# Kernel tuning notes

Hardware: AMD Instinct MI355X
Metric: run time of the kernel (lower is better)

Reference implementation:

```python
import jax, jax.numpy as jnp
import numpy as np
import math

N, L, S, H, E, D = 2, 2048, 2048, 16, 64, 64

def setup_inputs() -> dict:
    key = jax.random.key(0)
    kq, kk, kv = jax.random.split(key, 3)
    return {
        "queries": jax.random.normal(kq, (N, L, H, E), dtype=jnp.float32),
        "keys": jax.random.normal(kk, (N, S, H, E), dtype=jnp.float32),
        "values": jax.random.normal(kv, (N, S, H, D), dtype=jnp.float32),
        "attn_mask": jnp.zeros((L, S), dtype=jnp.float32),  # additive mask
    }

def reference(queries, keys, values, attn_mask):
    e = queries.shape[-1]
    softmax_temp = 1.0 / math.sqrt(e)  # self.softmax_temp is None -> 1/sqrt(E)
    # (N,L,H,E) x (N,S,H,E) -> (N,H,L,S)
    qk = jnp.einsum('nlhe,nshe->nhls', queries, keys)
    qk = qk + attn_mask  # additive mask broadcast over (N,H)
    att = jax.nn.softmax(softmax_temp * qk, axis=-1)
    # dropout rate 0.0 (eval) -> identity
    v = jnp.einsum('nhls,nshd->nlhd', att, values)
    return v
```

## Files before the change

### kernel.cpp

```cpp
#include <hip/hip_runtime.h>
#include <hip/hip_bf16.h>


typedef short bf16x8 __attribute__((ext_vector_type(8)));
typedef short short4v __attribute__((ext_vector_type(4)));
typedef unsigned uint2v __attribute__((ext_vector_type(2)));
typedef unsigned uint4v __attribute__((ext_vector_type(4)));
typedef float f32x4 __attribute__((ext_vector_type(4)));

constexpr int Nb = 2, Lq = 2048, Sk = 2048, Hh = 16, Ee = 64, Dd = 64;
constexpr int BM = 128;
constexpr int BN = 64;
constexpr int NT = Sk / BN;
constexpr int KVB = 4096;
constexpr int MSKB = 2048;
constexpr float SCALE_LOG2E = 0.125f * 1.4426950408889634f;

__device__ __forceinline__ short f2bf(float f) {
  union { float f; unsigned u; } v; v.f = f;
  unsigned r = (v.u + 0x7fffu + ((v.u >> 16) & 1u)) >> 16;
  return (short)r;
}

__device__ __forceinline__ unsigned pack_bf16x2(float a, float b) {
  union { __hip_bfloat162 h; unsigned u; } v;
  float2 f; f.x = a; f.y = b;
  v.h = __float22bfloat162_rn(f);
  return v.u;
}

__device__ __forceinline__ float bf_lo(unsigned u) { return __uint_as_float(u << 16); }
__device__ __forceinline__ float bf_hi(unsigned u) { return __uint_as_float(u & 0xffff0000u); }

__device__ __forceinline__ void async_copy16(const void* g, void* l) {
  __builtin_amdgcn_global_load_lds(
      (const __attribute__((address_space(1))) unsigned int*)g,
      (__attribute__((address_space(3))) unsigned int*)l, 16, 0, 0);
}

__global__ __launch_bounds__(256) void prep_all(const float* __restrict__ K,
                                                const float* __restrict__ V,
                                                const float* __restrict__ M,
                                                short* __restrict__ KVf,
                                                short* __restrict__ Mg) {
  if (blockIdx.x < KVB) {
    int gid = blockIdx.x * 256 + threadIdx.x;
    int off8 = gid & 1023;
    int t  = (gid >> 10) & 31;
    int nh = gid >> 15;
    int n = nh >> 4, h = nh & 15;
    short* dst = KVf + ((size_t)(nh * NT + t)) * 8192 + off8 * 8;
    if (off8 < 512) {
      int ch = off8 >> 6;
      int l  = off8 & 63;
      int sb = ch >> 1, kc = ch & 1, c = l & 15, quad = l >> 4;
      const float* p = K + (((size_t)n * Sk + (t * 64 + sb * 16 + c)) * Hh + h) * Ee
                         + kc * 32 + quad * 8;
      float4 x = *(const float4*)(p);
      float4 y = *(const float4*)(p + 4);
      bf16x8 o;
      o[0] = f2bf(x.x); o[1] = f2bf(x.y); o[2] = f2bf(x.z); o[3] = f2bf(x.w);
      o[4] = f2bf(y.x); o[5] = f2bf(y.y); o[6] = f2bf(y.z); o[7] = f2bf(y.w);
      *(bf16x8*)dst = o;
    } else {
      int pos = off8 - 512;
      int chunk = pos >> 6;
      int l = pos & 63;
      int db = chunk >> 1, sbp = chunk & 1, cc = l & 15, quad = l >> 4;
      const float* pbase = V + (((size_t)n * Sk + (t * 64 + sbp * 32 + quad * 4)) * Hh + h) * Dd
                             + db * 16 + cc;
      bf16x8 o;
#pragma unroll
      for (int k = 0; k < 8; ++k) {
        int s_off = (k >> 2) * 16 + (k & 3);
        o[k] = f2bf(pbase[(size_t)s_off * Hh * Dd]);
      }
      *(bf16x8*)dst = o;
    }
  } else {
    int u = (blockIdx.x - KVB) * 256 + threadIdx.x;
    int sub  = u & 3;
    int lane = (u >> 2) & 63;
    int t    = (u >> 8) & 31;
    int qw   = u >> 13;
    int cb = sub >> 1, sbp = sub & 1;
    int c = lane & 15, quad = lane >> 4;
    int row = (qw >> 2) * 128 + (qw & 3) * 32 + cb * 16 + c;
    short o[8];
#pragma unroll
    for (int k = 0; k < 2; ++k) {
      int sb = sbp * 2 + k;
      float4 mv = *(const float4*)(M + (size_t)row * Sk + t * 64 + sb * 16 + quad * 4);
      o[k * 4 + 0] = f2bf(mv.x * SCALE_LOG2E);
      o[k * 4 + 1] = f2bf(mv.y * SCALE_LOG2E);
      o[k * 4 + 2] = f2bf(mv.z * SCALE_LOG2E);
      o[k * 4 + 3] = f2bf(mv.w * SCALE_LOG2E);
    }
    *(bf16x8*)(Mg + (size_t)u * 8) = *(const bf16x8*)o;
  }
}

__global__ __launch_bounds__(256, 2) void attn_fwd(
    const float* __restrict__ Q, const short* __restrict__ KVf,
    const short* __restrict__ Mg, float* __restrict__ Out)
{
  __shared__ short KV[3][8192];

  const int tid  = threadIdx.x;
  const int lane = tid & 63;
  const int w    = tid >> 6;
  const int quad = lane >> 4;
  const int c    = lane & 15;

  const int id   = blockIdx.x;
  const int slot = id >> 3;
  const int nh   = (id & 7) * 4 + (slot & 3);
  const int qt   = (slot >> 2) & 15;
  const int n    = nh >> 4;
  const int h    = nh & 15;

  const int row0 = qt * BM + w * 32;
  constexpr int tc = NT;

  bf16x8 qfrag[2][2];
#pragma unroll
  for (int cb = 0; cb < 2; ++cb) {
    const float* qp = Q + (((size_t)n * Lq + (row0 + cb * 16 + c)) * Hh + h) * Ee;
#pragma unroll
    for (int kc = 0; kc < 2; ++kc) {
      const float* p = qp + kc * 32 + quad * 8;
      float4 x = *(const float4*)(p);
      float4 y = *(const float4*)(p + 4);
      bf16x8 f;
      f[0] = f2bf(x.x * SCALE_LOG2E); f[1] = f2bf(x.y * SCALE_LOG2E);
      f[2] = f2bf(x.z * SCALE_LOG2E); f[3] = f2bf(x.w * SCALE_LOG2E);
      f[4] = f2bf(y.x * SCALE_LOG2E); f[5] = f2bf(y.y * SCALE_LOG2E);
      f[6] = f2bf(y.z * SCALE_LOG2E); f[7] = f2bf(y.w * SCALE_LOG2E);
      qfrag[cb][kc] = f;
    }
  }

  f32x4 o[2][4];
#pragma unroll
  for (int cb = 0; cb < 2; ++cb)
#pragma unroll
    for (int db = 0; db < 4; ++db) { o[cb][db][0] = 0.f; o[cb][db][1] = 0.f; o[cb][db][2] = 0.f; o[cb][db][3] = 0.f; }
  float rs[2] = {0.f, 0.f};

  const short* kvt = KVf + (size_t)nh * NT * 8192;
  const short* mbase = Mg + (size_t)(qt * 4 + w) * 65536 + lane * 32;

  uint4v mcur[4];
#pragma unroll
  for (int i = 0; i < 4; ++i) mcur[i] = *(const uint4v*)(mbase + i * 8);
#pragma unroll
  for (int i = 0; i < 4; ++i) {
    int seg = w * 4 + i;
    async_copy16(kvt + seg * 512 + lane * 8, &KV[0][seg * 512 + lane * 8]);
  }
#pragma unroll
  for (int i = 0; i < 4; ++i) {
    int seg = w * 4 + i;
    async_copy16(kvt + 8192 + seg * 512 + lane * 8, &KV[1][seg * 512 + lane * 8]);
  }
  asm volatile("s_waitcnt vmcnt(4)" ::: "memory");
  __builtin_amdgcn_s_barrier();

  int bR = 0;
  for (int tt = 0; tt < tc; ++tt) {
    const short* kb = &KV[bR][0];

    f32x4 sacc[2][4];
#pragma unroll
    for (int cb = 0; cb < 2; ++cb)
#pragma unroll
      for (int sbp = 0; sbp < 2; ++sbp) {
        uint4v m = mcur[cb * 2 + sbp];
        sacc[cb][sbp * 2 + 0][0] = bf_lo(m.x); sacc[cb][sbp * 2 + 0][1] = bf_hi(m.x);
        sacc[cb][sbp * 2 + 0][2] = bf_lo(m.y); sacc[cb][sbp * 2 + 0][3] = bf_hi(m.y);
        sacc[cb][sbp * 2 + 1][0] = bf_lo(m.z); sacc[cb][sbp * 2 + 1][1] = bf_hi(m.z);
        sacc[cb][sbp * 2 + 1][2] = bf_lo(m.w); sacc[cb][sbp * 2 + 1][3] = bf_hi(m.w);
      }

    if (tt + 1 < tc) {
      const short* gm = mbase + (size_t)(tt + 1) * 2048;
#pragma unroll
      for (int i = 0; i < 4; ++i) mcur[i] = *(const uint4v*)(gm + i * 8);
    }
    if (tt + 2 < tc) {
      int bW = bR + 2; if (bW >= 3) bW -= 3;
      const short* gk = kvt + (size_t)(tt + 2) * 8192;
      short* lw = &KV[bW][0];
#pragma unroll
      for (int i = 0; i < 4; ++i) {
        int seg = w * 4 + i;
        async_copy16(gk + seg * 512 + lane * 8, &lw[seg * 512 + lane * 8]);
      }
    }

    short4v pv[2][4];
#pragma unroll
    for (int sb = 0; sb < 4; ++sb) {
      bf16x8 kf0 = *(const bf16x8*)&kb[(sb * 2 + 0) * 512 + lane * 8];
      bf16x8 kf1 = *(const bf16x8*)&kb[(sb * 2 + 1) * 512 + lane * 8];
#pragma unroll
      for (int cb = 0; cb < 2; ++cb) {
        sacc[cb][sb] = __builtin_amdgcn_mfma_f32_16x16x32_bf16(kf0, qfrag[cb][0], sacc[cb][sb], 0, 0, 0);
        sacc[cb][sb] = __builtin_amdgcn_mfma_f32_16x16x32_bf16(kf1, qfrag[cb][1], sacc[cb][sb], 0, 0, 0);
      }
      if (sb > 0) {
        const int sl = sb - 1;
#pragma unroll
        for (int cb = 0; cb < 2; ++cb) {
          float p0 = __builtin_amdgcn_exp2f(sacc[cb][sl][0]);
          float p1 = __builtin_amdgcn_exp2f(sacc[cb][sl][1]);
          float p2 = __builtin_amdgcn_exp2f(sacc[cb][sl][2]);
          float p3 = __builtin_amdgcn_exp2f(sacc[cb][sl][3]);
          rs[cb] += (p0 + p1) + (p2 + p3);
          union { uint2v u; short4v s; } uu;
          uu.u.x = pack_bf16x2(p0, p1);
          uu.u.y = pack_bf16x2(p2, p3);
          pv[cb][sl] = uu.s;
        }
      }
    }
#pragma unroll
    for (int cb = 0; cb < 2; ++cb) {
      float p0 = __builtin_amdgcn_exp2f(sacc[cb][3][0]);
      float p1 = __builtin_amdgcn_exp2f(sacc[cb][3][1]);
      float p2 = __builtin_amdgcn_exp2f(sacc[cb][3][2]);
      float p3 = __builtin_amdgcn_exp2f(sacc[cb][3][3]);
      rs[cb] += (p0 + p1) + (p2 + p3);
      union { uint2v u; short4v s; } uu;
      uu.u.x = pack_bf16x2(p0, p1);
      uu.u.y = pack_bf16x2(p2, p3);
      pv[cb][3] = uu.s;
    }

#pragma unroll
    for (int db = 0; db < 4; ++db) {
#pragma unroll
      for (int sbp = 0; sbp < 2; ++sbp) {
        bf16x8 vv = *(const bf16x8*)&kb[4096 + (db * 2 + sbp) * 512 + lane * 8];
        short4v v0, v1;
        v0[0] = vv[0]; v0[1] = vv[1]; v0[2] = vv[2]; v0[3] = vv[3];
        v1[0] = vv[4]; v1[1] = vv[5]; v1[2] = vv[6]; v1[3] = vv[7];
#pragma unroll
        for (int cb = 0; cb < 2; ++cb) {
          o[cb][db] = __builtin_amdgcn_mfma_f32_16x16x16bf16_1k(v0, pv[cb][sbp * 2 + 0], o[cb][db], 0, 0, 0);
          o[cb][db] = __builtin_amdgcn_mfma_f32_16x16x16bf16_1k(v1, pv[cb][sbp * 2 + 1], o[cb][db], 0, 0, 0);
        }
      }
    }

    asm volatile("s_waitcnt vmcnt(4)" ::: "memory");
    __builtin_amdgcn_s_barrier();
    bR += 1; if (bR == 3) bR = 0;
  }

#pragma unroll
  for (int cb = 0; cb < 2; ++cb) {
    float v = rs[cb];
    v += __shfl_xor(v, 16, 64);
    v += __shfl_xor(v, 32, 64);
    const float inv = 1.0f / v;
    const int qrow = row0 + cb * 16 + c;
    float* op = Out + (((size_t)n * Lq + qrow) * Hh + h) * Dd + quad * 4;
#pragma unroll
    for (int db = 0; db < 4; ++db) {
      float4 ov;
      ov.x = o[cb][db][0] * inv; ov.y = o[cb][db][1] * inv;
      ov.z = o[cb][db][2] * inv; ov.w = o[cb][db][3] * inv;
      *(float4*)(op + db * 16) = ov;
    }
  }
}

extern "C" void kernel_launch(void* const* d_in, const int* in_sizes, int n_in,
                              void* d_out, int out_size, void* d_ws, size_t ws_size,
                              hipStream_t stream) {
  const float* Q   = (const float*)d_in[0];
  const float* K   = (const float*)d_in[1];
  const float* V   = (const float*)d_in[2];
  const float* Msk = (const float*)d_in[3];
  float* Out = (float*)d_out;

  short* KVf = (short*)d_ws;
  short* Mg  = KVf + (size_t)8388608;

  prep_all<<<dim3(KVB + MSKB), dim3(256), 0, stream>>>(K, V, Msk, KVf, Mg);
  attn_fwd<<<dim3(512), dim3(256), 0, stream>>>(Q, KVf, Mg, Out);
}
```

Measured before the change: 151.1 us.

## Process two KV tiles per barrier with four-buffer LDS ping-pong

Replaces the triple-buffered one-tile-per-iteration loop with a loop that handles two key/value tiles per iteration, using four LDS buffers in two ping-pong pairs and two register mask buffers. This halves the number of block barriers and removes the manual vmcnt waits and ring-index arithmetic. Prefetch distance is now two tiles, issued as a pair. In exchange, LDS per block grows from 48KB to 64KB, which may limit occupancy at two blocks per CU. The barrier is now __syncthreads, which likely waits for all outstanding loads and so gives up some of the load overlap.

```diff
diff --git a/kernel.cpp b/kernel.cpp
--- a/kernel.cpp
+++ b/kernel.cpp
@@ -104,7 +104,7 @@
     const float* __restrict__ Q, const short* __restrict__ KVf,
     const short* __restrict__ Mg, float* __restrict__ Out)
 {
-  __shared__ short KV[3][8192];
+  __shared__ short KV[4][8192];
 
   const int tid  = threadIdx.x;
   const int lane = tid & 63;
@@ -120,7 +120,6 @@
   const int h    = nh & 15;
 
   const int row0 = qt * BM + w * 32;
-  constexpr int tc = NT;
 
   bf16x8 qfrag[2][2];
 #pragma unroll
@@ -150,47 +149,25 @@
   const short* kvt = KVf + (size_t)nh * NT * 8192;
   const short* mbase = Mg + (size_t)(qt * 4 + w) * 65536 + lane * 32;
 
-  uint4v mcur[4];
-#pragma unroll
-  for (int i = 0; i < 4; ++i) mcur[i] = *(const uint4v*)(mbase + i * 8);
-#pragma unroll
-  for (int i = 0; i < 4; ++i) {
-    int seg = w * 4 + i;
-    async_copy16(kvt + seg * 512 + lane * 8, &KV[0][seg * 512 + lane * 8]);
-  }
-#pragma unroll
-  for (int i = 0; i < 4; ++i) {
-    int seg = w * 4 + i;
-    async_copy16(kvt + 8192 + seg * 512 + lane * 8, &KV[1][seg * 512 + lane * 8]);
-  }
-  asm volatile("s_waitcnt vmcnt(4)" ::: "memory");
-  __builtin_amdgcn_s_barrier();
-
-  int bR = 0;
-  for (int tt = 0; tt < tc; ++tt) {
-    const short* kb = &KV[bR][0];
-
+  auto half_step = [&](const short* __restrict__ kb, uint4v (&mc)[4],
+                       int tnext, short* __restrict__ lw, bool pf) {
     f32x4 sacc[2][4];
 #pragma unroll
     for (int cb = 0; cb < 2; ++cb)
 #pragma unroll
       for (int sbp = 0; sbp < 2; ++sbp) {
-        uint4v m = mcur[cb * 2 + sbp];
+        uint4v m = mc[cb * 2 + sbp];
         sacc[cb][sbp * 2 + 0][0] = bf_lo(m.x); sacc[cb][sbp * 2 + 0][1] = bf_hi(m.x);
         sacc[cb][sbp * 2 + 0][2] = bf_lo(m.y); sacc[cb][sbp * 2 + 0][3] = bf_hi(m.y);
         sacc[cb][sbp * 2 + 1][0] = bf_lo(m.z); sacc[cb][sbp * 2 + 1][1] = bf_hi(m.z);
         sacc[cb][sbp * 2 + 1][2] = bf_lo(m.w); sacc[cb][sbp * 2 + 1][3] = bf_hi(m.w);
       }
 
-    if (tt + 1 < tc) {
-      const short* gm = mbase + (size_t)(tt + 1) * 2048;
-#pragma unroll
-      for (int i = 0; i < 4; ++i) mcur[i] = *(const uint4v*)(gm + i * 8);
-    }
-    if (tt + 2 < tc) {
-      int bW = bR + 2; if (bW >= 3) bW -= 3;
-      const short* gk = kvt + (size_t)(tt + 2) * 8192;
-      short* lw = &KV[bW][0];
+    if (pf) {
+      const short* gm = mbase + (size_t)tnext * 2048;
+#pragma unroll
+      for (int i = 0; i < 4; ++i) mc[i] = *(const uint4v*)(gm + i * 8);
+      const short* gk = kvt + (size_t)tnext * 8192;
 #pragma unroll
       for (int i = 0; i < 4; ++i) {
         int seg = w * 4 + i;
@@ -252,10 +229,29 @@
         }
       }
     }
-
-    asm volatile("s_waitcnt vmcnt(4)" ::: "memory");
-    __builtin_amdgcn_s_barrier();
-    bR += 1; if (bR == 3) bR = 0;
+  };
+
+  uint4v mcurA[4], mcurB[4];
+#pragma unroll
+  for (int i = 0; i < 4; ++i) {
+    mcurA[i] = *(const uint4v*)(mbase + i * 8);
+    mcurB[i] = *(const uint4v*)(mbase + 2048 + i * 8);
+  }
+#pragma unroll
+  for (int i = 0; i < 4; ++i) {
+    int seg = w * 4 + i;
+    async_copy16(kvt + seg * 512 + lane * 8, &KV[0][seg * 512 + lane * 8]);
+    async_copy16(kvt + 8192 + seg * 512 + lane * 8, &KV[1][seg * 512 + lane * 8]);
+  }
+  __syncthreads();
+
+  for (int kk = 0; kk < 16; ++kk) {
+    const int pr = (kk & 1) << 1;
+    const int pw = ((kk + 1) & 1) << 1;
+    const bool pf = (kk < 15);
+    half_step(&KV[pr][0],     mcurA, 2 * kk + 2, &KV[pw][0],     pf);
+    half_step(&KV[pr + 1][0], mcurB, 2 * kk + 3, &KV[pw + 1][0], pf);
+    __syncthreads();
   }
 
 #pragma unroll
```

Measured after the change: 153.4 us. About the same (+1.6%).

## Software-pipeline QK^T of next tile with PV of current tile using four LDS buffers

Applied to the files above, without the earlier changes.

Restructures the main loop so each step computes the QK^T scores and exp for tile t+1 while issuing the PV MFMAs for tile t, with a prologue and epilogue around it. The point is to hide the exp/softmax dependency latency behind independent MFMA work. To make this possible the LDS ring grows from three to four KV buffers, prefetch runs three tiles ahead, and mask loads run two tiles ahead with clamped indices. The cost is more LDS per block, which may limit the 2-blocks-per-CU occupancy, plus higher register pressure from the double P buffers and redundant clamped loads at the tail.

```diff
diff --git a/kernel.cpp b/kernel.cpp
--- a/kernel.cpp
+++ b/kernel.cpp
@@ -104,7 +104,7 @@
     const float* __restrict__ Q, const short* __restrict__ KVf,
     const short* __restrict__ Mg, float* __restrict__ Out)
 {
-  __shared__ short KV[3][8192];
+  __shared__ short KV[4][8192];
 
   const int tid  = threadIdx.x;
   const int lane = tid & 63;
@@ -120,7 +120,6 @@
   const int h    = nh & 15;
 
   const int row0 = qt * BM + w * 32;
-  constexpr int tc = NT;
 
   bf16x8 qfrag[2][2];
 #pragma unroll
@@ -151,6 +150,23 @@
   const short* mbase = Mg + (size_t)(qt * 4 + w) * 65536 + lane * 32;
 
   uint4v mcur[4];
+  short4v pvA[2][4], pvB[2][4];
+
+  auto exp_sb = [&](f32x4 (&sacc)[2][4], short4v (&pn)[2][4], int sl) {
+#pragma unroll
+    for (int cb = 0; cb < 2; ++cb) {
+      float p0 = __builtin_amdgcn_exp2f(sacc[cb][sl][0]);
+      float p1 = __builtin_amdgcn_exp2f(sacc[cb][sl][1]);
+      float p2 = __builtin_amdgcn_exp2f(sacc[cb][sl][2]);
+      float p3 = __builtin_amdgcn_exp2f(sacc[cb][sl][3]);
+      rs[cb] += (p0 + p1) + (p2 + p3);
+      union { uint2v u; short4v s; } uu;
+      uu.u.x = pack_bf16x2(p0, p1);
+      uu.u.y = pack_bf16x2(p2, p3);
+      pn[cb][sl] = uu.s;
+    }
+  };
+
 #pragma unroll
   for (int i = 0; i < 4; ++i) mcur[i] = *(const uint4v*)(mbase + i * 8);
 #pragma unroll
@@ -163,13 +179,10 @@
     int seg = w * 4 + i;
     async_copy16(kvt + 8192 + seg * 512 + lane * 8, &KV[1][seg * 512 + lane * 8]);
   }
-  asm volatile("s_waitcnt vmcnt(4)" ::: "memory");
+  asm volatile("s_waitcnt vmcnt(0)" ::: "memory");
   __builtin_amdgcn_s_barrier();
 
-  int bR = 0;
-  for (int tt = 0; tt < tc; ++tt) {
-    const short* kb = &KV[bR][0];
-
+  {
     f32x4 sacc[2][4];
 #pragma unroll
     for (int cb = 0; cb < 2; ++cb)
@@ -181,24 +194,14 @@
         sacc[cb][sbp * 2 + 1][0] = bf_lo(m.z); sacc[cb][sbp * 2 + 1][1] = bf_hi(m.z);
         sacc[cb][sbp * 2 + 1][2] = bf_lo(m.w); sacc[cb][sbp * 2 + 1][3] = bf_hi(m.w);
       }
-
-    if (tt + 1 < tc) {
-      const short* gm = mbase + (size_t)(tt + 1) * 2048;
-#pragma unroll
-      for (int i = 0; i < 4; ++i) mcur[i] = *(const uint4v*)(gm + i * 8);
-    }
-    if (tt + 2 < tc) {
-      int bW = bR + 2; if (bW >= 3) bW -= 3;
-      const short* gk = kvt + (size_t)(tt + 2) * 8192;
-      short* lw = &KV[bW][0];
-#pragma unroll
-      for (int i = 0; i < 4; ++i) {
-        int seg = w * 4 + i;
-        async_copy16(gk + seg * 512 + lane * 8, &lw[seg * 512 + lane * 8]);
-      }
-    }
-
-    short4v pv[2][4];
+#pragma unroll
+    for (int i = 0; i < 4; ++i) mcur[i] = *(const uint4v*)(mbase + 2048 + i * 8);
+#pragma unroll
+    for (int i = 0; i < 4; ++i) {
+      int seg = w * 4 + i;
+      async_copy16(kvt + 2 * 8192 + seg * 512 + lane * 8, &KV[2][seg * 512 + lane * 8]);
+    }
+    const short* kb = &KV[0][0];
 #pragma unroll
     for (int sb = 0; sb < 4; ++sb) {
       bf16x8 kf0 = *(const bf16x8*)&kb[(sb * 2 + 0) * 512 + lane * 8];
@@ -208,54 +211,95 @@
         sacc[cb][sb] = __builtin_amdgcn_mfma_f32_16x16x32_bf16(kf0, qfrag[cb][0], sacc[cb][sb], 0, 0, 0);
         sacc[cb][sb] = __builtin_amdgcn_mfma_f32_16x16x32_bf16(kf1, qfrag[cb][1], sacc[cb][sb], 0, 0, 0);
       }
-      if (sb > 0) {
-        const int sl = sb - 1;
-#pragma unroll
-        for (int cb = 0; cb < 2; ++cb) {
-          float p0 = __builtin_amdgcn_exp2f(sacc[cb][sl][0]);
-          float p1 = __builtin_amdgcn_exp2f(sacc[cb][sl][1]);
-          float p2 = __builtin_amdgcn_exp2f(sacc[cb][sl][2]);
-          float p3 = __builtin_amdgcn_exp2f(sacc[cb][sl][3]);
-          rs[cb] += (p0 + p1) + (p2 + p3);
-          union { uint2v u; short4v s; } uu;
-          uu.u.x = pack_bf16x2(p0, p1);
-          uu.u.y = pack_bf16x2(p2, p3);
-          pv[cb][sl] = uu.s;
+      if (sb > 0) exp_sb(sacc, pvA, sb - 1);
+    }
+    exp_sb(sacc, pvA, 3);
+  }
+
+  auto step = [&](int t, short4v (&pcur)[2][4], short4v (&pnxt)[2][4]) {
+    const short* kbP = &KV[t & 3][0];
+    const short* kbQ = &KV[(t + 1) & 3][0];
+
+    f32x4 sacc[2][4];
+#pragma unroll
+    for (int cb = 0; cb < 2; ++cb)
+#pragma unroll
+      for (int sbp = 0; sbp < 2; ++sbp) {
+        uint4v m = mcur[cb * 2 + sbp];
+        sacc[cb][sbp * 2 + 0][0] = bf_lo(m.x); sacc[cb][sbp * 2 + 0][1] = bf_hi(m.x);
+        sacc[cb][sbp * 2 + 0][2] = bf_lo(m.y); sacc[cb][sbp * 2 + 0][3] = bf_hi(m.y);
+        sacc[cb][sbp * 2 + 1][0] = bf_lo(m.z); sacc[cb][sbp * 2 + 1][1] = bf_hi(m.z);
+        sacc[cb][sbp * 2 + 1][2] = bf_lo(m.w); sacc[cb][sbp * 2 + 1][3] = bf_hi(m.w);
+      }
+
+    int tm = t + 2; if (tm > 31) tm = 31;
+    const short* gm = mbase + (size_t)tm * 2048;
+#pragma unroll
+    for (int i = 0; i < 4; ++i) mcur[i] = *(const uint4v*)(gm + i * 8);
+    int ts = t + 3; if (ts > 31) ts = 31;
+    const short* gk = kvt + (size_t)ts * 8192;
+    short* lw = &KV[(t + 3) & 3][0];
+#pragma unroll
+    for (int i = 0; i < 4; ++i) {
+      int seg = w * 4 + i;
+      async_copy16(gk + seg * 512 + lane * 8, &lw[seg * 512 + lane * 8]);
+    }
+
+#pragma unroll
+    for (int sb = 0; sb < 4; ++sb) {
+      bf16x8 kf0 = *(const bf16x8*)&kbQ[(sb * 2 + 0) * 512 + lane * 8];
+      bf16x8 kf1 = *(const bf16x8*)&kbQ[(sb * 2 + 1) * 512 + lane * 8];
+#pragma unroll
+      for (int cb = 0; cb < 2; ++cb) {
+        sacc[cb][sb] = __builtin_amdgcn_mfma_f32_16x16x32_bf16(kf0, qfrag[cb][0], sacc[cb][sb], 0, 0, 0);
+        sacc[cb][sb] = __builtin_amdgcn_mfma_f32_16x16x32_bf16(kf1, qfrag[cb][1], sacc[cb][sb], 0, 0, 0);
+      }
+      {
+        const int db = sb;
+#pragma unroll
+        for (int sbp = 0; sbp < 2; ++sbp) {
+          bf16x8 vv = *(const bf16x8*)&kbP[4096 + (db * 2 + sbp) * 512 + lane * 8];
+          short4v v0, v1;
+          v0[0] = vv[0]; v0[1] = vv[1]; v0[2] = vv[2]; v0[3] = vv[3];
+          v1[0] = vv[4]; v1[1] = vv[5]; v1[2] = vv[6]; v1[3] = vv[7];
+#pragma unroll
+          for (int cb = 0; cb < 2; ++cb) {
+            o[cb][db] = __builtin_amdgcn_mfma_f32_16x16x16bf16_1k(v0, pcur[cb][sbp * 2 + 0], o[cb][db], 0, 0, 0);
+            o[cb][db] = __builtin_amdgcn_mfma_f32_16x16x16bf16_1k(v1, pcur[cb][sbp * 2 + 1], o[cb][db], 0, 0, 0);
+          }
         }
       }
-    }
-#pragma unroll
-    for (int cb = 0; cb < 2; ++cb) {
-      float p0 = __builtin_amdgcn_exp2f(sacc[cb][3][0]);
-      float p1 = __builtin_amdgcn_exp2f(sacc[cb][3][1]);
-      float p2 = __builtin_amdgcn_exp2f(sacc[cb][3][2]);
-      float p3 = __builtin_amdgcn_exp2f(sacc[cb][3][3]);
-      rs[cb] += (p0 + p1) + (p2 + p3);
-      union { uint2v u; short4v s; } uu;
-      uu.u.x = pack_bf16x2(p0, p1);
-      uu.u.y = pack_bf16x2(p2, p3);
-      pv[cb][3] = uu.s;
-    }
-
+      if (sb > 0) exp_sb(sacc, pnxt, sb - 1);
+    }
+    exp_sb(sacc, pnxt, 3);
+
+    asm volatile("s_waitcnt vmcnt(8)" ::: "memory");
+    __builtin_amdgcn_s_barrier();
+  };
+
+  for (int p = 0; p < 15; ++p) {
+    step(2 * p,     pvA, pvB);
+    step(2 * p + 1, pvB, pvA);
+  }
+  step(30, pvA, pvB);
+
+  {
+    const short* kbP = &KV[3][0];
 #pragma unroll
     for (int db = 0; db < 4; ++db) {
 #pragma unroll
       for (int sbp = 0; sbp < 2; ++sbp) {
-        bf16x8 vv = *(const bf16x8*)&kb[4096 + (db * 2 + sbp) * 512 + lane * 8];
+        bf16x8 vv = *(const bf16x8*)&kbP[4096 + (db * 2 + sbp) * 512 + lane * 8];
         short4v v0, v1;
         v0[0] = vv[0]; v0[1] = vv[1]; v0[2] = vv[2]; v0[3] = vv[3];
         v1[0] = vv[4]; v1[1] = vv[5]; v1[2] = vv[6]; v1[3] = vv[7];
 #pragma unroll
         for (int cb = 0; cb < 2; ++cb) {
-          o[cb][db] = __builtin_amdgcn_mfma_f32_16x16x16bf16_1k(v0, pv[cb][sbp * 2 + 0], o[cb][db], 0, 0, 0);
-          o[cb][db] = __builtin_amdgcn_mfma_f32_16x16x16bf16_1k(v1, pv[cb][sbp * 2 + 1], o[cb][db], 0, 0, 0);
+          o[cb][db] = __builtin_amdgcn_mfma_f32_16x16x16bf16_1k(v0, pvB[cb][sbp * 2 + 0], o[cb][db], 0, 0, 0);
+          o[cb][db] = __builtin_amdgcn_mfma_f32_16x16x16bf16_1k(v1, pvB[cb][sbp * 2 + 1], o[cb][db], 0, 0, 0);
         }
       }
     }
-
-    asm volatile("s_waitcnt vmcnt(4)" ::: "memory");
-    __builtin_amdgcn_s_barrier();
-    bR += 1; if (bR == 3) bR = 0;
   }
 
 #pragma unroll
```

New measurement: 151.5 us. No clear change (+0.3%).
